# Kernel optimization log

Measured on AMD Instinct MI355X. Metric: run time of the kernel, lower is better.

Reference implementation:

```python
import jax, jax.numpy as jnp
import numpy as np

# Model dims (see init_kwargs / shape_source)
ROWS, COLS, C, K, L = 16, 16, 16, 3, 2
B, T = 16, 128
D = ROWS * COLS * C  # state_dim = 4096
PAD = (K - 1) // 2


def setup_inputs() -> dict:
    key = jax.random.key(0)
    ks = jax.random.split(key, 1 + 5 * L)
    inp = {"x_flat": jax.random.normal(ks[0], (B, T, ROWS * COLS), jnp.float32)}
    ki = 1
    for l in range(L):
        cin = (1 if l == 0 else C) + C  # conv sees concat(input, h)
        inp[f"conv_w{l}"] = jax.random.normal(ks[ki], (4 * C, cin, K), jnp.float32) * float(1.0 / np.sqrt(cin * K)); ki += 1
        inp[f"conv_b{l}"] = jnp.zeros((4 * C,), jnp.float32)
        s = float(1.0 / np.sqrt(D))
        inp[f"wq{l}"] = jax.random.normal(ks[ki], (D, D), jnp.float32) * s; ki += 1
        inp[f"wk{l}"] = jax.random.normal(ks[ki], (D, D), jnp.float32) * s; ki += 1
        inp[f"wv{l}"] = jax.random.normal(ks[ki], (D, D), jnp.float32) * s; ki += 1
        inp[f"wo{l}"] = jax.random.normal(ks[ki], (2 * D, D), jnp.float32) * float(1.0 / np.sqrt(2 * D)); ki += 1
    return inp


def _cell_step(x, h, c, cw, cb):
    # x: (B, ROWS, cin_x, COLS); h, c: (B, ROWS, C, COLS). Row-shared Conv1d
    # along cols over concat(x, h) -> 4C gates (standard ConvLSTM).
    z = jnp.concatenate([x, h], axis=2)
    z = z.reshape(B * ROWS, z.shape[2], COLS)
    g = jax.lax.conv_general_dilated(
        z, cw, window_strides=(1,), padding=[(PAD, PAD)],
        dimension_numbers=("NCH", "OIH", "NCH"))
    g = g.reshape(B, ROWS, 4 * C, COLS) + cb[None, None, :, None]
    i, f, gg, o = jnp.split(g, 4, axis=2)
    c_new = jax.nn.sigmoid(f) * c + jax.nn.sigmoid(i) * jnp.tanh(gg)
    h_new = jax.nn.sigmoid(o) * jnp.tanh(c_new)
    return h_new, c_new


def _attn_step(h_vec, kbuf, vbuf, step, wq, wo):
    # Causal dot-product attention: query from raw state, keys from raw
    # history, values from refined history (projections cached in kbuf/vbuf).
    q = h_vec @ wq                                        # (B, D)
    scores = jnp.einsum("bd,tbd->bt", q, kbuf) * (1.0 / np.sqrt(D))
    mask = (jnp.arange(T)[None, :] < step)                # (1, T) strictly-past
    scores = jnp.where(mask, scores, -1e30)
    m = jnp.max(scores, axis=1, keepdims=True)
    e = jnp.exp(scores - m) * mask
    w = e / jnp.maximum(e.sum(axis=1, keepdims=True), 1e-9)
    ctx = jnp.einsum("bt,tbd->bd", w, vbuf)               # zeros at step 0
    out = jnp.tanh(jnp.concatenate([h_vec, ctx], axis=1) @ wo)
    return out, w


def _forward(x_flat, layer_params):
    # frames: (T, B, ROWS, 1, COLS) -- matches torch view+unsqueeze(3)
    x = x_flat.reshape(B, T, ROWS, 1, COLS).transpose(1, 0, 2, 3, 4)
    h0 = tuple(jnp.zeros((B, ROWS, C, COLS), x_flat.dtype) for _ in range(L))
    kb0 = tuple(jnp.zeros((T, B, D), x_flat.dtype) for _ in range(L))

    def body(carry, x_t):
        hs, cs, kbs, vbs, s = carry
        inp = x_t
        nh, nc, nk, nv = [], [], [], []
        out = None
        for l in range(L):
            cw, cb, wq, wk, wv, wo = layer_params[l]
            h_raw, c_new = _cell_step(inp, hs[l], cs[l], cw, cb)
            h_vec = h_raw.reshape(B, D)
            out, _w = _attn_step(h_vec, kbs[l], vbs[l], s, wq, wo)
            nk.append(kbs[l].at[s].set(h_vec @ wk))   # append raw key
            nv.append(vbs[l].at[s].set(out @ wv))     # append refined value
            nh.append(h_raw); nc.append(c_new)
            inp = out.reshape(B, ROWS, C, COLS)
        return (tuple(nh), tuple(nc), tuple(nk), tuple(nv), s + 1), out

    init = (h0, h0, kb0, kb0, jnp.int32(0))
    _, outs = jax.lax.scan(body, init, x)
    return outs.transpose(1, 0, 2)  # (B, T, D) encoder outputs


def reference(x_flat, conv_w0, conv_b0, wq0, wk0, wv0, wo0,
              conv_w1, conv_b1, wq1, wk1, wv1, wo1):
    layer_params = [
        (conv_w0, conv_b0, wq0, wk0, wv0, wo0),
        (conv_w1, conv_b1, wq1, wk1, wv1, wo1),
    ]
    return _forward(x_flat, layer_params)
```

## Files before the change

kernel.cpp:

```cpp
#include <hip/hip_runtime.h>

typedef unsigned short u16;
typedef unsigned int u32;
typedef __attribute__((ext_vector_type(8))) short short8v;
typedef __attribute__((ext_vector_type(4))) float f32x4;
typedef __attribute__((ext_vector_type(8))) u16 ush8;
typedef __attribute__((ext_vector_type(4))) u16 ush4;

__device__ __forceinline__ u16 f2bf(float x) {
  u32 u = __builtin_bit_cast(u32, x);
  return (u16)((u + 0x7FFFu + ((u >> 16) & 1u)) >> 16);
}
__device__ __forceinline__ float bf2f(u16 h) {
  u32 u = ((u32)h) << 16;
  return __builtin_bit_cast(float, u);
}
__device__ __forceinline__ float sigm(float x) { return 1.f / (1.f + expf(-x)); }

typedef const __attribute__((address_space(1))) void gv_t;
typedef __attribute__((address_space(3))) void lv_t;
__device__ __forceinline__ void gload16(const void* g, void* l) {
  __builtin_amdgcn_global_load_lds((gv_t*)g, (lv_t*)l, 16, 0, 0);
}

__device__ __forceinline__ u32 ldsc32(const u32* p) {
  u32 v;
  asm volatile("global_load_dword %0, %1, off sc0 sc1\n\ts_waitcnt vmcnt(0)"
               : "=v"(v) : "v"(p) : "memory");
  return v;
}
__device__ __forceinline__ void atomswap32(u32* p, u32 v) {
  asm volatile("global_atomic_swap %0, %1, off" :: "v"(p), "v"(v) : "memory");
}

__global__ __launch_bounds__(256) void k_conv(int cin, int xmode,
    const float* __restrict__ xin, const float* __restrict__ cw,
    const float* __restrict__ cb, u16* __restrict__ hhi, u16* __restrict__ hlo)
{
  __shared__ float zb[32 * 18];
  __shared__ __align__(16) float wb[6144];
  __shared__ float bb[64];
  const int tid = threadIdx.x;
  const int b = blockIdx.x >> 4, r = blockIdx.x & 15;
  const int ch = tid >> 4, col = tid & 15;
  const int cx = cin - 16;
  for (int i = tid; i < 64 * cin * 3; i += 256) {
    int tap = i % 3, tmp = i / 3;
    int ic = tmp % cin, oc = tmp / cin;
    wb[(((oc & 15) * cin + ic) * 3 + tap) * 4 + (oc >> 4)] = cw[i];
  }
  if (tid < 64) bb[tid] = cb[tid];
  for (int i = tid; i < cin * 18; i += 256) zb[i] = 0.f;
  __syncthreads();
  float h = 0.f, c = 0.f;
  const int lane = tid & 63;
  for (int t = 0; t < 128; ++t) {
    if (xmode == 0) {
      if (ch == 0) zb[col + 1] = xin[((long)b * 128 + t) * 256 + r * 16 + col];
    } else {
      zb[ch * 18 + col + 1] = xin[((long)t * 16 + b) * 4096 + r * 256 + ch * 16 + col];
    }
    zb[(cx + ch) * 18 + col + 1] = h;
    __syncthreads();
    float a0 = bb[ch], a1 = bb[16 + ch], a2 = bb[32 + ch], a3 = bb[48 + ch];
    for (int ic = 0; ic < cin; ++ic) {
      float z1 = zb[ic * 18 + col + 1];
      float z0 = __shfl(z1, lane - 1);
      float z2 = __shfl(z1, lane + 1);
      if (col == 0) z0 = 0.f;
      if (col == 15) z2 = 0.f;
      const float4* wp = (const float4*)&wb[(ch * cin + ic) * 12];
      float4 w0 = wp[0], w1 = wp[1], w2 = wp[2];
      a0 += z0 * w0.x + z1 * w1.x + z2 * w2.x;
      a1 += z0 * w0.y + z1 * w1.y + z2 * w2.y;
      a2 += z0 * w0.z + z1 * w1.z + z2 * w2.z;
      a3 += z0 * w0.w + z1 * w1.w + z2 * w2.w;
    }
    __syncthreads();
    c = sigm(a1) * c + sigm(a0) * tanhf(a2);
    h = sigm(a3) * tanhf(c);
    long idx = ((long)t * 16 + b) * 4096 + (long)r * 256 + ch * 16 + col;
    u16 hh = f2bf(h);
    hhi[idx] = hh;
    hlo[idx] = f2bf(h - bf2f(hh));
  }
}

__global__ __launch_bounds__(256) void k_tsplit3(
    const float* __restrict__ W0, const float* __restrict__ W1,
    const float* __restrict__ W2, u16* __restrict__ hi, u16* __restrict__ lo)
{
  __shared__ float tb[32][33];
  const int y = blockIdx.y;
  const float* W = (y == 0) ? W0 : (y == 1) ? W1 : W2;
  u16* hid = hi + (unsigned long)y * 16777216UL;
  u16* lod = lo + (unsigned long)y * 16777216UL;
  const int tn = blockIdx.x & 127, tk = blockIdx.x >> 7;
  const int n0 = tn * 32, k0 = tk * 32;
  const int lr = threadIdx.x >> 5, lc = threadIdx.x & 31;
  #pragma unroll
  for (int i = 0; i < 4; ++i)
    tb[lr + i * 8][lc] = W[(long)(k0 + lr + i * 8) * 4096 + n0 + lc];
  __syncthreads();
  #pragma unroll
  for (int i = 0; i < 4; ++i) {
    int n = lr + i * 8;
    float v = tb[lc][n];
    long idx = (long)(n0 + n) * 4096 + k0 + lc;
    u16 h = f2bf(v);
    hid[idx] = h;
    lod[idx] = f2bf(v - bf2f(h));
  }
}

__global__ __launch_bounds__(256) void k_prepB2(
    const float* __restrict__ Woc, const float* __restrict__ Wv,
    u16* __restrict__ thi, u16* __restrict__ tlo,
    u16* __restrict__ vhi, u16* __restrict__ vlo)
{
  if (blockIdx.y == 1) {
    long i = ((long)blockIdx.x * 256 + threadIdx.x) * 4;
    const float4 v = *(const float4*)&Wv[i];
    u16 h0 = f2bf(v.x), h1 = f2bf(v.y), h2 = f2bf(v.z), h3 = f2bf(v.w);
    ush4 hv = {h0, h1, h2, h3};
    ush4 lv = {f2bf(v.x - bf2f(h0)), f2bf(v.y - bf2f(h1)),
               f2bf(v.z - bf2f(h2)), f2bf(v.w - bf2f(h3))};
    *(ush4*)&vhi[i] = hv;
    *(ush4*)&vlo[i] = lv;
    return;
  }
  __shared__ float tb[32][33];
  const int tn = blockIdx.x & 127, tk = blockIdx.x >> 7;
  const int n0 = tn * 32, k0 = tk * 32;
  const int lr = threadIdx.x >> 5, lc = threadIdx.x & 31;
  #pragma unroll
  for (int i = 0; i < 4; ++i)
    tb[lr + i * 8][lc] = Woc[(long)(k0 + lr + i * 8) * 4096 + n0 + lc];
  __syncthreads();
  #pragma unroll
  for (int i = 0; i < 4; ++i) {
    int n = lr + i * 8;
    float v = tb[lc][n];
    long idx = (long)(n0 + n) * 4096 + k0 + lc;
    u16 h = f2bf(v);
    thi[idx] = h;
    tlo[idx] = f2bf(v - bf2f(h));
  }
}

__global__ __launch_bounds__(256) void k_scores(
    const u16* __restrict__ Ahi, long lda, long aBS,
    const u16* __restrict__ Bhi, long ldb, long bBS,
    float* __restrict__ Sp)
{
  __shared__ __align__(16) u16 lds[2][16384];
  const int tid = threadIdx.x;
  const int lane = tid & 63;
  const int wv = tid >> 6;
  const long aOff = (long)blockIdx.y * aBS;
  const long bOff = (long)blockIdx.y * bBS;
  const long cOff = (long)blockIdx.y * 16384 + (long)blockIdx.z * 262144;
  const int kbase = blockIdx.z * 512;

  const int l8 = lane >> 3;
  const int cslot = (lane & 7) ^ l8;
  const int ck = (cslot & 3) * 8;
  const u16* aSrc = Ahi + aOff + (wv * 32 + l8) * lda + ck;
  const u16* bSrc = Bhi + bOff + (wv * 32 + l8) * ldb + ck;
  const int ldsAo = wv * 2048;
  const int ldsBo = 8192 + wv * 2048;

  const int r15 = lane & 15, kq = lane >> 4;
  const int s7 = r15 & 7;
  const int oHi = (kq ^ s7) * 8;
  const int aQ = (wv >> 1) * 64;
  const int bQ = (wv & 1) * 64;

  f32x4 acc[4][4] = {};

#define STAGE(buf, kofs)                                                     \
  {                                                                          \
    const u16* sa = aSrc + (kofs);                                           \
    const u16* sb = bSrc + (kofs);                                           \
    u16* la = &lds[buf][ldsAo];                                              \
    u16* lb = &lds[buf][ldsBo];                                              \
    gload16(sa,            la);        gload16(sa +  8 * lda, la + 512);     \
    gload16(sa + 16 * lda, la + 1024); gload16(sa + 24 * lda, la + 1536);    \
    gload16(sb,            lb);        gload16(sb +  8 * ldb, lb + 512);     \
    gload16(sb + 16 * ldb, lb + 1024); gload16(sb + 24 * ldb, lb + 1536);    \
  }

  STAGE(0, kbase)
  __syncthreads();
  int cur = 0;
  for (int k0 = kbase; k0 < kbase + 512; k0 += 32) {
    if (k0 + 32 < kbase + 512) STAGE(cur ^ 1, k0 + 32)
    const u16* L = &lds[cur][0];
    short8v bh[4];
    #pragma unroll
    for (int j = 0; j < 4; ++j)
      bh[j] = *(const short8v*)&L[8192 + (bQ + j * 16 + r15) * 64 + oHi];
    #pragma unroll
    for (int i = 0; i < 4; ++i) {
      short8v ah = *(const short8v*)&L[(aQ + i * 16 + r15) * 64 + oHi];
      #pragma unroll
      for (int j = 0; j < 4; ++j)
        acc[i][j] = __builtin_amdgcn_mfma_f32_16x16x32_bf16(ah, bh[j], acc[i][j], 0, 0, 0);
    }
    __syncthreads();
    cur ^= 1;
  }
#undef STAGE
  const long row0 = aQ, col0 = bQ;
  #pragma unroll
  for (int i = 0; i < 4; ++i)
    #pragma unroll
    for (int j = 0; j < 4; ++j) {
      long rr = row0 + i * 16 + kq * 4;
      long cc = col0 + j * 16 + r15;
      #pragma unroll
      for (int g = 0; g < 4; ++g)
        Sp[cOff + (rr + g) * 128 + cc] = acc[i][j][g];
    }
}

template<int NM, bool LOOUT>
__global__ __launch_bounds__(512) void k_gemm256(
    const u16* __restrict__ Ahi, const u16* __restrict__ Alo,
    const u16* __restrict__ Bhi, const u16* __restrict__ Blo,
    u16* __restrict__ Chi, u16* __restrict__ Clo, long ldc, int nTc)
{
  __shared__ __align__(16) u16 lds[73728];
  const int tid = threadIdx.x, lane = tid & 63, wv = tid >> 6;
  const int nwg = gridDim.x;
  const int bid2 = (blockIdx.x & 7) * (nwg >> 3) + (blockIdx.x >> 3);
  const int nT = bid2 % nTc, mT = bid2 / nTc;
  const long aRow0 = (long)mT * 256, bRow0 = (long)nT * 128;

  const int l8 = lane >> 3, cslot = (lane & 7) ^ l8, ck = (cslot & 3) * 8;
  const u16* aSrc = ((cslot < 4) ? Ahi : Alo) + (aRow0 + wv * 32 + l8) * 4096 + ck;
  const u16* bSrc = ((cslot < 4) ? Bhi : Blo) + (bRow0 + wv * 16 + l8) * 4096 + ck;
  const int laO = wv * 2048;
  const int lbO = 16384 + wv * 1024;

  const int r15 = lane & 15, kq = lane >> 4, s7 = r15 & 7;
  const int oHi = (kq ^ s7) * 8, oLo = ((4 + kq) ^ s7) * 8;
  const int wm = wv >> 1, wn = wv & 1;
  f32x4 acc[4][4] = {};

#define STG(buf, kofs)                                                       \
  {                                                                          \
    const u16* sa = aSrc + (kofs);                                           \
    const u16* sb = bSrc + (kofs);                                           \
    u16* la = &lds[(buf) * 24576 + laO];                                     \
    u16* lb = &lds[(buf) * 24576 + lbO];                                     \
    gload16(sa,             la);       gload16(sa +  8 * 4096, la + 512);    \
    gload16(sa + 16 * 4096, la + 1024); gload16(sa + 24 * 4096, la + 1536);  \
    gload16(sb,             lb);       gload16(sb +  8 * 4096, lb + 512);    \
  }

  STG(0, 0) STG(1, 32)
  for (int kt = 0; kt < 128; ++kt) {
    if (kt < 127) { asm volatile("s_waitcnt vmcnt(6)" ::: "memory"); }
    else          { asm volatile("s_waitcnt vmcnt(0)" ::: "memory"); }
    __builtin_amdgcn_sched_barrier(0);
    __builtin_amdgcn_s_barrier();
    const int bb = (kt % 3) * 24576;
    if (kt < 126) STG((kt + 2) % 3, (kt + 2) * 32)
    short8v ah[4], al[4], bh[4], bl[4];
    #pragma unroll
    for (int j = 0; j < 4; ++j) {
      int rb = bb + 16384 + (wn * 64 + j * 16 + r15) * 64;
      bh[j] = *(const short8v*)&lds[rb + oHi];
      if (NM >= 3) bl[j] = *(const short8v*)&lds[rb + oLo];
    }
    #pragma unroll
    for (int i = 0; i < 4; ++i) {
      int ra = bb + (wm * 64 + i * 16 + r15) * 64;
      ah[i] = *(const short8v*)&lds[ra + oHi];
      if (NM >= 2) al[i] = *(const short8v*)&lds[ra + oLo];
    }
    #pragma unroll
    for (int i = 0; i < 4; ++i)
      #pragma unroll
      for (int j = 0; j < 4; ++j) {
        acc[i][j] = __builtin_amdgcn_mfma_f32_16x16x32_bf16(ah[i], bh[j], acc[i][j], 0, 0, 0);
        if (NM >= 3) acc[i][j] = __builtin_amdgcn_mfma_f32_16x16x32_bf16(ah[i], bl[j], acc[i][j], 0, 0, 0);
        if (NM >= 2) acc[i][j] = __builtin_amdgcn_mfma_f32_16x16x32_bf16(al[i], bh[j], acc[i][j], 0, 0, 0);
      }
  }
#undef STG
  const long row0 = aRow0 + wm * 64;
  const long col0 = bRow0 + wn * 64;
  #pragma unroll
  for (int i = 0; i < 4; ++i)
    #pragma unroll
    for (int j = 0; j < 4; ++j) {
      long rr = row0 + i * 16 + kq * 4;
      long cc = col0 + j * 16 + r15;
      #pragma unroll
      for (int g = 0; g < 4; ++g) {
        float v = acc[i][j][g];
        long idx = (rr + g) * ldc + cc;
        u16 h = f2bf(v);
        Chi[idx] = h;
        if (LOOUT) Clo[idx] = f2bf(v - bf2f(h));
      }
    }
}

__global__ __launch_bounds__(256) void k_softmax(const float* __restrict__ Sp,
    float* __restrict__ Wx, u32* __restrict__ flags)
{
  if (blockIdx.x == 0) atomswap32(&flags[threadIdx.x * 16], 0);
  const int wv = threadIdx.x >> 6, lane = threadIdx.x & 63;
  const int idx = blockIdx.x * 4 + wv;
  const int b = idx >> 7, t = idx & 127;
  const float* row = &Sp[(long)idx * 128];
  float s0 = 0.f, s1 = 0.f;
  #pragma unroll
  for (int s = 0; s < 8; ++s) {
    s0 += row[s * 262144 + lane];
    s1 += row[s * 262144 + lane + 64];
  }
  float v0 = (lane < t) ? s0 * 0.015625f : -1e30f;
  float v1 = (lane + 64 < t) ? s1 * 0.015625f : -1e30f;
  float m = fmaxf(v0, v1);
  #pragma unroll
  for (int off = 32; off; off >>= 1) m = fmaxf(m, __shfl_xor(m, off));
  float e0 = (lane < t) ? expf(v0 - m) : 0.f;
  float e1 = (lane + 64 < t) ? expf(v1 - m) : 0.f;
  float s = e0 + e1;
  #pragma unroll
  for (int off = 32; off; off >>= 1) s += __shfl_xor(s, off);
  float inv = 1.f / fmaxf(s, 1e-9f);
  float* wr = &Wx[((long)t * 16 + b) * 128];
  wr[lane] = e0 * inv;
  wr[lane + 64] = e1 * inv;
}

__global__ __launch_bounds__(512) void k_phaseC(
    const u16* __restrict__ Wvh, const u16* __restrict__ Wvl,
    const float* __restrict__ Wx,
    const u16* __restrict__ hoh, const u16* __restrict__ hol,
    u16* __restrict__ ring_h,
    float* __restrict__ fdest, int dmode, u32* __restrict__ flags)
{
  __shared__ float VO_lds[128 * 256];
  __shared__ float vo_w[8][256];
  __shared__ float pctx0[256], pctx1[256];
  const int tid = threadIdx.x;
  const int lane = tid & 63, wv = tid >> 6;
  const int n0 = blockIdx.x * 16;
  const int r15 = lane & 15, kq = lane >> 4;
  const long kb = (long)wv * 512 + kq * 8;

  short8v Bh[16], Bl[16];
  {
    const u16* bh = Wvh + (long)(n0 + r15) * 4096 + kb;
    const u16* bl = Wvl + (long)(n0 + r15) * 4096 + kb;
    #pragma unroll
    for (int c = 0; c < 16; ++c) {
      Bh[c] = *(const short8v*)(bh + c * 32);
      Bl[c] = *(const short8v*)(bl + c * 32);
    }
    #pragma unroll
    for (int c = 0; c < 16; ++c) {
      asm volatile("" : "+v"(Bh[c]));
      asm volatile("" : "+v"(Bl[c]));
    }
  }
  const long abase = (long)r15 * 4096 + kb;
  const int b8 = tid >> 4, col8 = tid & 15;

#define GBAR_PCTX(n, T)                                                      \
  {                                                                          \
    asm volatile("s_waitcnt vmcnt(0)" ::: "memory");                         \
    __syncthreads();                                                         \
    if (tid == 0) atomswap32(&flags[(u32)blockIdx.x * 16], (n));             \
    if (tid >= 256) {                                                        \
      const int id = tid - 256;                                              \
      const int bm = id >> 4;                                                \
      const float* wrowm = &Wx[((long)((T) + 1) * 16 + bm) * 128];           \
      float c0 = 0.f, c1 = 0.f;                                              \
      int tp = 0;                                                            \
      for (; tp + 1 < (T); tp += 2) {                                        \
        c0 += wrowm[tp] * VO_lds[tp * 256 + id];                             \
        c1 += wrowm[tp + 1] * VO_lds[(tp + 1) * 256 + id];                   \
      }                                                                      \
      if (tp < (T)) c0 += wrowm[tp] * VO_lds[tp * 256 + id];                 \
      pctx0[id] = c0; pctx1[id] = c1;                                        \
    } else {                                                                 \
      while (ldsc32(&flags[tid * 16]) < (n)) __builtin_amdgcn_s_sleep(1);    \
    }                                                                        \
    __syncthreads();                                                         \
  }

#define RING_STORE(slot, oval)                                               \
  {                                                                          \
    u16 hh_ = f2bf(oval);                                                    \
    u32 vh_ = hh_;                                                           \
    u32 ph_ = (u32)__shfl_xor((int)vh_, 1);                                  \
    if (!(col8 & 1)) {                                                       \
      long oi_ = (long)(slot) * 65536 + (long)b8 * 4096 + n0 + col8;         \
      atomswap32((u32*)&ring_h[oi_], vh_ | (ph_ << 16));                     \
    }                                                                        \
  }

  if (tid < 256) {
    float v = tanhf(bf2f(hoh[(long)b8 * 12288 + n0 + col8])
                  + bf2f(hol[(long)b8 * 12288 + n0 + col8]));
    RING_STORE(0, v)
    if (dmode == 0) fdest[(long)b8 * 4096 + n0 + col8] = v;
    else            fdest[(long)b8 * 128 * 4096 + n0 + col8] = v;
  }
  u32 bn = 1;
  GBAR_PCTX(bn, 0) ++bn;

#define MF(a, b) acc = __builtin_amdgcn_mfma_f32_16x16x32_bf16(a, b, acc, 0, 0, 0);

  for (int t = 0; t < 127; ++t) {
    const u16* ph = ring_h + (long)t * 65536 + abase;
    short8v xh[16];
    #pragma unroll
    for (int c = 0; c < 16; ++c) xh[c] = *(const short8v*)(ph + c * 32);
    f32x4 acc = {0.f, 0.f, 0.f, 0.f};
    #pragma unroll
    for (int c = 0; c < 16; ++c) { MF(xh[c], Bh[c]) MF(xh[c], Bl[c]) }
    #pragma unroll
    for (int g = 0; g < 4; ++g)
      vo_w[wv][(kq * 4 + g) * 16 + r15] = acc[g];
    __syncthreads();
    if (tid < 256) {
      float v = vo_w[0][tid] + vo_w[1][tid] + vo_w[2][tid] + vo_w[3][tid]
              + vo_w[4][tid] + vo_w[5][tid] + vo_w[6][tid] + vo_w[7][tid];
      VO_lds[t * 256 + tid] = v;
      const float* wrow = &Wx[((long)(t + 1) * 16 + b8) * 128];
      long hix = ((long)(t + 1) * 16 + b8) * 12288 + n0 + col8;
      float o = tanhf(bf2f(hoh[hix]) + bf2f(hol[hix])
                      + pctx0[tid] + pctx1[tid] + wrow[t] * v);
      RING_STORE(t + 1, o)
      if (dmode == 0) fdest[((long)(t + 1) * 16 + b8) * 4096 + n0 + col8] = o;
      else            fdest[((long)b8 * 128 + (t + 1)) * 4096 + n0 + col8] = o;
    }
    if (t < 126) { GBAR_PCTX(bn, t + 1) ++bn; }
  }
#undef GBAR_PCTX
#undef RING_STORE
#undef MF
}

extern "C" void kernel_launch(void* const* d_in, const int* in_sizes, int n_in,
                              void* d_out, int out_size, void* d_ws, size_t ws_size,
                              hipStream_t stream)
{
  (void)in_sizes; (void)n_in; (void)out_size;
  if (ws_size < 472383488UL) return;
  char* ws = (char*)d_ws;
  u16* WT_hi = (u16*)(ws + 0UL);
  u16* WT_lo = (u16*)(ws + 100663296UL);
  u16* WV_hi = (u16*)(ws + 33554432UL);
  u16* WV_lo = (u16*)(ws + 134217728UL);
  u16* QKOh  = (u16*)(ws + 201326592UL);
  u16* QKOl  = (u16*)(ws + 251658240UL);
  u16* Wvo_hi = (u16*)(ws + 301989888UL);
  u16* Wvo_lo = (u16*)(ws + 335544320UL);
  u16* Hs_hi = (u16*)(ws + 369098752UL);
  u16* Hs_lo = (u16*)(ws + 385875968UL);
  float* Wmx  = (float*)(ws + 403701760UL);
  float* OUT0 = (float*)(ws + 404754432UL);
  u16* ring_h = (u16*)(ws + 438308864UL);
  float* Sp   = (float*)(ws + 455086080UL);
  u32* flg    = (u32*)(ws + 471859200UL);
  float* dout = (float*)d_out;
  const float* x_flat = (const float*)d_in[0];

  for (int l = 0; l < 2; ++l) {
    const float* cw = (const float*)d_in[1 + l * 6];
    const float* cb = (const float*)d_in[2 + l * 6];
    const float* wq = (const float*)d_in[3 + l * 6];
    const float* wk = (const float*)d_in[4 + l * 6];
    const float* wv = (const float*)d_in[5 + l * 6];
    const float* wo = (const float*)d_in[6 + l * 6];
    const int cin = (l == 0) ? 17 : 32;

    hipLaunchKernelGGL(k_conv, dim3(256), dim3(256), 0, stream,
        cin, l, (l == 0) ? x_flat : OUT0, cw, cb, Hs_hi, Hs_lo);

    hipLaunchKernelGGL(k_tsplit3, dim3(16384, 3), dim3(256), 0, stream,
        wq, wk, wo, WT_hi, WT_lo);
    hipLaunchKernelGGL((k_gemm256<1, false>), dim3(512), dim3(512), 0, stream,
        Hs_hi, Hs_hi, WT_hi, WT_hi, QKOh, (u16*)nullptr, 12288L, 64);
    hipLaunchKernelGGL((k_gemm256<3, true>), dim3(256), dim3(512), 0, stream,
        Hs_hi, Hs_lo, WT_hi + 33554432UL, WT_lo + 33554432UL,
        QKOh + 8192, QKOl + 8192, 12288L, 32);

    hipLaunchKernelGGL(k_prepB2, dim3(16384, 2), dim3(256), 0, stream,
        wo + 16777216UL, wv, WT_hi, WT_lo, WV_hi, WV_lo);
    hipLaunchKernelGGL((k_gemm256<2, true>), dim3(512), dim3(512), 0, stream,
        WT_hi, WT_lo, WV_hi, WV_hi, Wvo_hi, Wvo_lo, 4096L, 32);

    hipLaunchKernelGGL(k_scores, dim3(1, 16, 8), dim3(256), 0, stream,
        QKOh, 12288L, 196608L, QKOh + 4096, 12288L, 196608L, Sp);
    hipLaunchKernelGGL(k_softmax, dim3(512), dim3(256), 0, stream, Sp, Wmx, flg);

    hipLaunchKernelGGL(k_phaseC, dim3(256), dim3(512), 0, stream,
        Wvo_hi, Wvo_lo, Wmx, QKOh + 8192, QKOl + 8192,
        ring_h, (l == 0) ? OUT0 : dout, l, flg);
  }
}
```

Baseline: 4.083 ms.

## Fuse conv and weight-prep kernels, merge three GEMMs into one launch

Runs the ConvLSTM recurrence and all weight transpose/bf16-split preprocessing in a single k_prep launch, with the serial conv blocks (low indices) overlapping the bandwidth-bound weight conversion. The three hi/lo bf16 GEMMs are combined into one k_gemmB launch dispatched by block index. Unused lo halves of Wq/Wk/Wv are no longer written, and the HO lo buffer is compacted to a 4096 stride, which cuts memory traffic and workspace. The cost is a very large heterogeneous grid where the 256 long-running conv blocks may become the tail. OUT0 and Sp now share the same workspace region, which relies on OUT0 being fully consumed before k_scores writes Sp.

```diff
diff --git a/kernel.cpp b/kernel.cpp
--- a/kernel.cpp
+++ b/kernel.cpp
@@ -33,71 +33,101 @@
   asm volatile("global_atomic_swap %0, %1, off" :: "v"(p), "v"(v) : "memory");
 }
 
-__global__ __launch_bounds__(256) void k_conv(int cin, int xmode,
-    const float* __restrict__ xin, const float* __restrict__ cw,
-    const float* __restrict__ cb, u16* __restrict__ hhi, u16* __restrict__ hlo)
-{
-  __shared__ float zb[32 * 18];
-  __shared__ __align__(16) float wb[6144];
-  __shared__ float bb[64];
+__global__ __launch_bounds__(256) void k_prep(int cin, int xmode,
+    const float* __restrict__ xin,
+    const float* __restrict__ cw, const float* __restrict__ cb,
+    const float* __restrict__ wq, const float* __restrict__ wk,
+    const float* __restrict__ wo, const float* __restrict__ wv,
+    u16* __restrict__ hhi, u16* __restrict__ hlo,
+    u16* __restrict__ WT_hi, u16* __restrict__ WTh_lo,
+    u16* __restrict__ WTc_hi, u16* __restrict__ WTc_lo,
+    u16* __restrict__ WV_hi)
+{
+  __shared__ __align__(16) float smem[6912];
+  const int bx = blockIdx.x;
   const int tid = threadIdx.x;
-  const int b = blockIdx.x >> 4, r = blockIdx.x & 15;
-  const int ch = tid >> 4, col = tid & 15;
-  const int cx = cin - 16;
-  for (int i = tid; i < 64 * cin * 3; i += 256) {
-    int tap = i % 3, tmp = i / 3;
-    int ic = tmp % cin, oc = tmp / cin;
-    wb[(((oc & 15) * cin + ic) * 3 + tap) * 4 + (oc >> 4)] = cw[i];
-  }
-  if (tid < 64) bb[tid] = cb[tid];
-  for (int i = tid; i < cin * 18; i += 256) zb[i] = 0.f;
-  __syncthreads();
-  float h = 0.f, c = 0.f;
-  const int lane = tid & 63;
-  for (int t = 0; t < 128; ++t) {
-    if (xmode == 0) {
-      if (ch == 0) zb[col + 1] = xin[((long)b * 128 + t) * 256 + r * 16 + col];
-    } else {
-      zb[ch * 18 + col + 1] = xin[((long)t * 16 + b) * 4096 + r * 256 + ch * 16 + col];
-    }
-    zb[(cx + ch) * 18 + col + 1] = h;
+
+  if (bx < 256) {
+    float* zb = smem;
+    float* wb = smem + 576;
+    float* bb = smem + 6720;
+    const int b = bx >> 4, r = bx & 15;
+    const int ch = tid >> 4, col = tid & 15;
+    const int cx = cin - 16;
+    for (int i = tid; i < 64 * cin * 3; i += 256) {
+      int tap = i % 3, tmp = i / 3;
+      int ic = tmp % cin, oc = tmp / cin;
+      wb[(((oc & 15) * cin + ic) * 3 + tap) * 4 + (oc >> 4)] = cw[i];
+    }
+    if (tid < 64) bb[tid] = cb[tid];
+    for (int i = tid; i < cin * 18; i += 256) zb[i] = 0.f;
     __syncthreads();
-    float a0 = bb[ch], a1 = bb[16 + ch], a2 = bb[32 + ch], a3 = bb[48 + ch];
-    for (int ic = 0; ic < cin; ++ic) {
-      float z1 = zb[ic * 18 + col + 1];
-      float z0 = __shfl(z1, lane - 1);
-      float z2 = __shfl(z1, lane + 1);
-      if (col == 0) z0 = 0.f;
-      if (col == 15) z2 = 0.f;
-      const float4* wp = (const float4*)&wb[(ch * cin + ic) * 12];
-      float4 w0 = wp[0], w1 = wp[1], w2 = wp[2];
-      a0 += z0 * w0.x + z1 * w1.x + z2 * w2.x;
-      a1 += z0 * w0.y + z1 * w1.y + z2 * w2.y;
-      a2 += z0 * w0.z + z1 * w1.z + z2 * w2.z;
-      a3 += z0 * w0.w + z1 * w1.w + z2 * w2.w;
-    }
-    __syncthreads();
-    c = sigm(a1) * c + sigm(a0) * tanhf(a2);
-    h = sigm(a3) * tanhf(c);
-    long idx = ((long)t * 16 + b) * 4096 + (long)r * 256 + ch * 16 + col;
-    u16 hh = f2bf(h);
-    hhi[idx] = hh;
-    hlo[idx] = f2bf(h - bf2f(hh));
-  }
-}
-
-__global__ __launch_bounds__(256) void k_tsplit3(
-    const float* __restrict__ W0, const float* __restrict__ W1,
-    const float* __restrict__ W2, u16* __restrict__ hi, u16* __restrict__ lo)
-{
-  __shared__ float tb[32][33];
-  const int y = blockIdx.y;
-  const float* W = (y == 0) ? W0 : (y == 1) ? W1 : W2;
-  u16* hid = hi + (unsigned long)y * 16777216UL;
-  u16* lod = lo + (unsigned long)y * 16777216UL;
-  const int tn = blockIdx.x & 127, tk = blockIdx.x >> 7;
+    float h = 0.f, c = 0.f;
+    const int lane = tid & 63;
+    for (int t = 0; t < 128; ++t) {
+      if (xmode == 0) {
+        if (ch == 0) zb[col + 1] = xin[((long)b * 128 + t) * 256 + r * 16 + col];
+      } else {
+        zb[ch * 18 + col + 1] = xin[((long)t * 16 + b) * 4096 + r * 256 + ch * 16 + col];
+      }
+      zb[(cx + ch) * 18 + col + 1] = h;
+      __syncthreads();
+      float a0 = bb[ch], a1 = bb[16 + ch], a2 = bb[32 + ch], a3 = bb[48 + ch];
+      for (int ic = 0; ic < cin; ++ic) {
+        float z1 = zb[ic * 18 + col + 1];
+        float z0 = __shfl(z1, lane - 1);
+        float z2 = __shfl(z1, lane + 1);
+        if (col == 0) z0 = 0.f;
+        if (col == 15) z2 = 0.f;
+        const float4* wp = (const float4*)&wb[(ch * cin + ic) * 12];
+        float4 w0 = wp[0], w1 = wp[1], w2 = wp[2];
+        a0 += z0 * w0.x + z1 * w1.x + z2 * w2.x;
+        a1 += z0 * w0.y + z1 * w1.y + z2 * w2.y;
+        a2 += z0 * w0.z + z1 * w1.z + z2 * w2.z;
+        a3 += z0 * w0.w + z1 * w1.w + z2 * w2.w;
+      }
+      __syncthreads();
+      c = sigm(a1) * c + sigm(a0) * tanhf(a2);
+      h = sigm(a3) * tanhf(c);
+      long idx = ((long)t * 16 + b) * 4096 + (long)r * 256 + ch * 16 + col;
+      u16 hh = f2bf(h);
+      hhi[idx] = hh;
+      hlo[idx] = f2bf(h - bf2f(hh));
+    }
+    return;
+  }
+
+  if (bx >= 65792) {
+    long i = ((long)(bx - 65792) * 256 + tid) * 4;
+    const float4 v = *(const float4*)&wv[i];
+    ush4 hv = {f2bf(v.x), f2bf(v.y), f2bf(v.z), f2bf(v.w)};
+    *(ush4*)&WV_hi[i] = hv;
+    return;
+  }
+
+  float (*tb)[33] = (float(*)[33])smem;
+  const float* W;
+  u16 *hid, *lod;
+  int writeLo;
+  int tile;
+  if (bx < 49408) {
+    int t = bx - 256;
+    int y = t >> 14;
+    tile = t & 16383;
+    W = (y == 0) ? wq : (y == 1) ? wk : wo;
+    hid = WT_hi + (unsigned long)y * 16777216UL;
+    lod = WTh_lo;
+    writeLo = (y == 2);
+  } else {
+    tile = bx - 49408;
+    W = wo + 16777216UL;
+    hid = WTc_hi;
+    lod = WTc_lo;
+    writeLo = 1;
+  }
+  const int tn = tile & 127, tk = tile >> 7;
   const int n0 = tn * 32, k0 = tk * 32;
-  const int lr = threadIdx.x >> 5, lc = threadIdx.x & 31;
+  const int lr = tid >> 5, lc = tid & 31;
   #pragma unroll
   for (int i = 0; i < 4; ++i)
     tb[lr + i * 8][lc] = W[(long)(k0 + lr + i * 8) * 4096 + n0 + lc];
@@ -109,42 +139,113 @@
     long idx = (long)(n0 + n) * 4096 + k0 + lc;
     u16 h = f2bf(v);
     hid[idx] = h;
-    lod[idx] = f2bf(v - bf2f(h));
-  }
-}
-
-__global__ __launch_bounds__(256) void k_prepB2(
-    const float* __restrict__ Woc, const float* __restrict__ Wv,
-    u16* __restrict__ thi, u16* __restrict__ tlo,
-    u16* __restrict__ vhi, u16* __restrict__ vlo)
-{
-  if (blockIdx.y == 1) {
-    long i = ((long)blockIdx.x * 256 + threadIdx.x) * 4;
-    const float4 v = *(const float4*)&Wv[i];
-    u16 h0 = f2bf(v.x), h1 = f2bf(v.y), h2 = f2bf(v.z), h3 = f2bf(v.w);
-    ush4 hv = {h0, h1, h2, h3};
-    ush4 lv = {f2bf(v.x - bf2f(h0)), f2bf(v.y - bf2f(h1)),
-               f2bf(v.z - bf2f(h2)), f2bf(v.w - bf2f(h3))};
-    *(ush4*)&vhi[i] = hv;
-    *(ush4*)&vlo[i] = lv;
-    return;
-  }
-  __shared__ float tb[32][33];
-  const int tn = blockIdx.x & 127, tk = blockIdx.x >> 7;
-  const int n0 = tn * 32, k0 = tk * 32;
-  const int lr = threadIdx.x >> 5, lc = threadIdx.x & 31;
+    if (writeLo) lod[idx] = f2bf(v - bf2f(h));
+  }
+}
+
+template<int NM, bool LOOUT>
+__device__ __forceinline__ void gemm_core(u16* lds, int bid, int nwg,
+    const u16* __restrict__ Ahi, const u16* __restrict__ Alo,
+    const u16* __restrict__ Bhi, const u16* __restrict__ Blo,
+    u16* __restrict__ Chi, u16* __restrict__ Clo,
+    long ldc, long ldclo, int nTc)
+{
+  const int tid = threadIdx.x, lane = tid & 63, wv = tid >> 6;
+  const int bid2 = (bid & 7) * (nwg >> 3) + (bid >> 3);
+  const int nT = bid2 % nTc, mT = bid2 / nTc;
+  const long aRow0 = (long)mT * 256, bRow0 = (long)nT * 128;
+
+  const int l8 = lane >> 3, cslot = (lane & 7) ^ l8, ck = (cslot & 3) * 8;
+  const u16* aSrc = ((cslot < 4) ? Ahi : Alo) + (aRow0 + wv * 32 + l8) * 4096 + ck;
+  const u16* bSrc = ((cslot < 4) ? Bhi : Blo) + (bRow0 + wv * 16 + l8) * 4096 + ck;
+  const int laO = wv * 2048;
+  const int lbO = 16384 + wv * 1024;
+
+  const int r15 = lane & 15, kq = lane >> 4, s7 = r15 & 7;
+  const int oHi = (kq ^ s7) * 8, oLo = ((4 + kq) ^ s7) * 8;
+  const int wm = wv >> 1, wn = wv & 1;
+  f32x4 acc[4][4] = {};
+
+#define STG(buf, kofs)                                                       \
+  {                                                                          \
+    const u16* sa = aSrc + (kofs);                                           \
+    const u16* sb = bSrc + (kofs);                                           \
+    u16* la = &lds[(buf) * 24576 + laO];                                     \
+    u16* lb = &lds[(buf) * 24576 + lbO];                                     \
+    gload16(sa,             la);       gload16(sa +  8 * 4096, la + 512);    \
+    gload16(sa + 16 * 4096, la + 1024); gload16(sa + 24 * 4096, la + 1536);  \
+    gload16(sb,             lb);       gload16(sb +  8 * 4096, lb + 512);    \
+  }
+
+  STG(0, 0) STG(1, 32)
+  for (int kt = 0; kt < 128; ++kt) {
+    if (kt < 127) { asm volatile("s_waitcnt vmcnt(6)" ::: "memory"); }
+    else          { asm volatile("s_waitcnt vmcnt(0)" ::: "memory"); }
+    __builtin_amdgcn_sched_barrier(0);
+    __builtin_amdgcn_s_barrier();
+    const int bb = (kt % 3) * 24576;
+    if (kt < 126) STG((kt + 2) % 3, (kt + 2) * 32)
+    short8v ah[4], al[4], bh[4], bl[4];
+    #pragma unroll
+    for (int j = 0; j < 4; ++j) {
+      int rb = bb + 16384 + (wn * 64 + j * 16 + r15) * 64;
+      bh[j] = *(const short8v*)&lds[rb + oHi];
+      if (NM >= 3) bl[j] = *(const short8v*)&lds[rb + oLo];
+    }
+    #pragma unroll
+    for (int i = 0; i < 4; ++i) {
+      int ra = bb + (wm * 64 + i * 16 + r15) * 64;
+      ah[i] = *(const short8v*)&lds[ra + oHi];
+      if (NM >= 2) al[i] = *(const short8v*)&lds[ra + oLo];
+    }
+    #pragma unroll
+    for (int i = 0; i < 4; ++i)
+      #pragma unroll
+      for (int j = 0; j < 4; ++j) {
+        acc[i][j] = __builtin_amdgcn_mfma_f32_16x16x32_bf16(ah[i], bh[j], acc[i][j], 0, 0, 0);
+        if (NM >= 3) acc[i][j] = __builtin_amdgcn_mfma_f32_16x16x32_bf16(ah[i], bl[j], acc[i][j], 0, 0, 0);
+        if (NM >= 2) acc[i][j] = __builtin_amdgcn_mfma_f32_16x16x32_bf16(al[i], bh[j], acc[i][j], 0, 0, 0);
+      }
+  }
+#undef STG
+  const long row0 = aRow0 + wm * 64;
+  const long col0 = bRow0 + wn * 64;
   #pragma unroll
   for (int i = 0; i < 4; ++i)
-    tb[lr + i * 8][lc] = Woc[(long)(k0 + lr + i * 8) * 4096 + n0 + lc];
-  __syncthreads();
-  #pragma unroll
-  for (int i = 0; i < 4; ++i) {
-    int n = lr + i * 8;
-    float v = tb[lc][n];
-    long idx = (long)(n0 + n) * 4096 + k0 + lc;
-    u16 h = f2bf(v);
-    thi[idx] = h;
-    tlo[idx] = f2bf(v - bf2f(h));
+    #pragma unroll
+    for (int j = 0; j < 4; ++j) {
+      long rr = row0 + i * 16 + kq * 4;
+      long cc = col0 + j * 16 + r15;
+      #pragma unroll
+      for (int g = 0; g < 4; ++g) {
+        float v = acc[i][j][g];
+        u16 h = f2bf(v);
+        Chi[(rr + g) * ldc + cc] = h;
+        if (LOOUT) Clo[(rr + g) * ldclo + cc] = f2bf(v - bf2f(h));
+      }
+    }
+}
+
+__global__ __launch_bounds__(512) void k_gemmB(
+    const u16* __restrict__ Hs_hi, const u16* __restrict__ Hs_lo,
+    const u16* __restrict__ WT_hi, const u16* __restrict__ WTh_lo,
+    const u16* __restrict__ WTc_hi, const u16* __restrict__ WTc_lo,
+    const u16* __restrict__ WV_hi,
+    u16* __restrict__ QKOh, u16* __restrict__ HOlo,
+    u16* __restrict__ Wvo_hi, u16* __restrict__ Wvo_lo)
+{
+  __shared__ __align__(16) u16 lds[73728];
+  const int bx = blockIdx.x;
+  if (bx < 512) {
+    gemm_core<1, false>(lds, bx, 512, Hs_hi, Hs_hi, WT_hi, WT_hi,
+                        QKOh, (u16*)nullptr, 12288L, 0L, 64);
+  } else if (bx < 768) {
+    gemm_core<3, true>(lds, bx - 512, 256, Hs_hi, Hs_lo,
+                       WT_hi + 33554432UL, WTh_lo,
+                       QKOh + 8192, HOlo, 12288L, 4096L, 32);
+  } else {
+    gemm_core<2, true>(lds, bx - 768, 512, WTc_hi, WTc_lo, WV_hi, WV_hi,
+                       Wvo_hi, Wvo_lo, 4096L, 4096L, 32);
   }
 }
 
@@ -221,91 +322,6 @@
       #pragma unroll
       for (int g = 0; g < 4; ++g)
         Sp[cOff + (rr + g) * 128 + cc] = acc[i][j][g];
-    }
-}
-
-template<int NM, bool LOOUT>
-__global__ __launch_bounds__(512) void k_gemm256(
-    const u16* __restrict__ Ahi, const u16* __restrict__ Alo,
-    const u16* __restrict__ Bhi, const u16* __restrict__ Blo,
-    u16* __restrict__ Chi, u16* __restrict__ Clo, long ldc, int nTc)
-{
-  __shared__ __align__(16) u16 lds[73728];
-  const int tid = threadIdx.x, lane = tid & 63, wv = tid >> 6;
-  const int nwg = gridDim.x;
-  const int bid2 = (blockIdx.x & 7) * (nwg >> 3) + (blockIdx.x >> 3);
-  const int nT = bid2 % nTc, mT = bid2 / nTc;
-  const long aRow0 = (long)mT * 256, bRow0 = (long)nT * 128;
-
-  const int l8 = lane >> 3, cslot = (lane & 7) ^ l8, ck = (cslot & 3) * 8;
-  const u16* aSrc = ((cslot < 4) ? Ahi : Alo) + (aRow0 + wv * 32 + l8) * 4096 + ck;
-  const u16* bSrc = ((cslot < 4) ? Bhi : Blo) + (bRow0 + wv * 16 + l8) * 4096 + ck;
-  const int laO = wv * 2048;
-  const int lbO = 16384 + wv * 1024;
-
-  const int r15 = lane & 15, kq = lane >> 4, s7 = r15 & 7;
-  const int oHi = (kq ^ s7) * 8, oLo = ((4 + kq) ^ s7) * 8;
-  const int wm = wv >> 1, wn = wv & 1;
-  f32x4 acc[4][4] = {};
-
-#define STG(buf, kofs)                                                       \
-  {                                                                          \
-    const u16* sa = aSrc + (kofs);                                           \
-    const u16* sb = bSrc + (kofs);                                           \
-    u16* la = &lds[(buf) * 24576 + laO];                                     \
-    u16* lb = &lds[(buf) * 24576 + lbO];                                     \
-    gload16(sa,             la);       gload16(sa +  8 * 4096, la + 512);    \
-    gload16(sa + 16 * 4096, la + 1024); gload16(sa + 24 * 4096, la + 1536);  \
-    gload16(sb,             lb);       gload16(sb +  8 * 4096, lb + 512);    \
-  }
-
-  STG(0, 0) STG(1, 32)
-  for (int kt = 0; kt < 128; ++kt) {
-    if (kt < 127) { asm volatile("s_waitcnt vmcnt(6)" ::: "memory"); }
-    else          { asm volatile("s_waitcnt vmcnt(0)" ::: "memory"); }
-    __builtin_amdgcn_sched_barrier(0);
-    __builtin_amdgcn_s_barrier();
-    const int bb = (kt % 3) * 24576;
-    if (kt < 126) STG((kt + 2) % 3, (kt + 2) * 32)
-    short8v ah[4], al[4], bh[4], bl[4];
-    #pragma unroll
-    for (int j = 0; j < 4; ++j) {
-      int rb = bb + 16384 + (wn * 64 + j * 16 + r15) * 64;
-      bh[j] = *(const short8v*)&lds[rb + oHi];
-      if (NM >= 3) bl[j] = *(const short8v*)&lds[rb + oLo];
-    }
-    #pragma unroll
-    for (int i = 0; i < 4; ++i) {
-      int ra = bb + (wm * 64 + i * 16 + r15) * 64;
-      ah[i] = *(const short8v*)&lds[ra + oHi];
-      if (NM >= 2) al[i] = *(const short8v*)&lds[ra + oLo];
-    }
-    #pragma unroll
-    for (int i = 0; i < 4; ++i)
-      #pragma unroll
-      for (int j = 0; j < 4; ++j) {
-        acc[i][j] = __builtin_amdgcn_mfma_f32_16x16x32_bf16(ah[i], bh[j], acc[i][j], 0, 0, 0);
-        if (NM >= 3) acc[i][j] = __builtin_amdgcn_mfma_f32_16x16x32_bf16(ah[i], bl[j], acc[i][j], 0, 0, 0);
-        if (NM >= 2) acc[i][j] = __builtin_amdgcn_mfma_f32_16x16x32_bf16(al[i], bh[j], acc[i][j], 0, 0, 0);
-      }
-  }
-#undef STG
-  const long row0 = aRow0 + wm * 64;
-  const long col0 = bRow0 + wn * 64;
-  #pragma unroll
-  for (int i = 0; i < 4; ++i)
-    #pragma unroll
-    for (int j = 0; j < 4; ++j) {
-      long rr = row0 + i * 16 + kq * 4;
-      long cc = col0 + j * 16 + r15;
-      #pragma unroll
-      for (int g = 0; g < 4; ++g) {
-        float v = acc[i][j][g];
-        long idx = (rr + g) * ldc + cc;
-        u16 h = f2bf(v);
-        Chi[idx] = h;
-        if (LOOUT) Clo[idx] = f2bf(v - bf2f(h));
-      }
     }
 }
 
@@ -409,7 +425,7 @@
 
   if (tid < 256) {
     float v = tanhf(bf2f(hoh[(long)b8 * 12288 + n0 + col8])
-                  + bf2f(hol[(long)b8 * 12288 + n0 + col8]));
+                  + bf2f(hol[(long)b8 * 4096 + n0 + col8]));
     RING_STORE(0, v)
     if (dmode == 0) fdest[(long)b8 * 4096 + n0 + col8] = v;
     else            fdest[(long)b8 * 128 * 4096 + n0 + col8] = v;
@@ -436,9 +452,9 @@
               + vo_w[4][tid] + vo_w[5][tid] + vo_w[6][tid] + vo_w[7][tid];
       VO_lds[t * 256 + tid] = v;
       const float* wrow = &Wx[((long)(t + 1) * 16 + b8) * 128];
-      long hix = ((long)(t + 1) * 16 + b8) * 12288 + n0 + col8;
-      float o = tanhf(bf2f(hoh[hix]) + bf2f(hol[hix])
-                      + pctx0[tid] + pctx1[tid] + wrow[t] * v);
+      float ho = bf2f(hoh[((long)(t + 1) * 16 + b8) * 12288 + n0 + col8])
+               + bf2f(hol[((long)(t + 1) * 16 + b8) * 4096 + n0 + col8]);
+      float o = tanhf(ho + pctx0[tid] + pctx1[tid] + wrow[t] * v);
       RING_STORE(t + 1, o)
       if (dmode == 0) fdest[((long)(t + 1) * 16 + b8) * 4096 + n0 + col8] = o;
       else            fdest[((long)b8 * 128 + (t + 1)) * 4096 + n0 + col8] = o;
@@ -455,23 +471,24 @@
                               hipStream_t stream)
 {
   (void)in_sizes; (void)n_in; (void)out_size;
-  if (ws_size < 472383488UL) return;
+  if (ws_size < 454049792UL) return;
   char* ws = (char*)d_ws;
-  u16* WT_hi = (u16*)(ws + 0UL);
-  u16* WT_lo = (u16*)(ws + 100663296UL);
-  u16* WV_hi = (u16*)(ws + 33554432UL);
-  u16* WV_lo = (u16*)(ws + 134217728UL);
-  u16* QKOh  = (u16*)(ws + 201326592UL);
-  u16* QKOl  = (u16*)(ws + 251658240UL);
+  u16* WT_hi  = (u16*)(ws + 0UL);
+  u16* WTh_lo = (u16*)(ws + 100663296UL);
+  u16* WTc_hi = (u16*)(ws + 134217728UL);
+  u16* WTc_lo = (u16*)(ws + 167772160UL);
+  u16* WV_hi  = (u16*)(ws + 201326592UL);
+  u16* QKOh   = (u16*)(ws + 234881024UL);
+  u16* HOlo   = (u16*)(ws + 285212672UL);
   u16* Wvo_hi = (u16*)(ws + 301989888UL);
   u16* Wvo_lo = (u16*)(ws + 335544320UL);
-  u16* Hs_hi = (u16*)(ws + 369098752UL);
-  u16* Hs_lo = (u16*)(ws + 385875968UL);
-  float* Wmx  = (float*)(ws + 403701760UL);
-  float* OUT0 = (float*)(ws + 404754432UL);
-  u16* ring_h = (u16*)(ws + 438308864UL);
-  float* Sp   = (float*)(ws + 455086080UL);
-  u32* flg    = (u32*)(ws + 471859200UL);
+  u16* Hs_hi  = (u16*)(ws + 369098752UL);
+  u16* Hs_lo  = (u16*)(ws + 385875968UL);
+  float* Wmx  = (float*)(ws + 402653184UL);
+  u16* ring_h = (u16*)(ws + 403701760UL);
+  float* OUT0 = (float*)(ws + 420478976UL);
+  float* Sp   = (float*)(ws + 420478976UL);
+  u32* flg    = (u32*)(ws + 454033408UL);
   float* dout = (float*)d_out;
   const float* x_flat = (const float*)d_in[0];
 
@@ -484,28 +501,20 @@
     const float* wo = (const float*)d_in[6 + l * 6];
     const int cin = (l == 0) ? 17 : 32;
 
-    hipLaunchKernelGGL(k_conv, dim3(256), dim3(256), 0, stream,
-        cin, l, (l == 0) ? x_flat : OUT0, cw, cb, Hs_hi, Hs_lo);
-
-    hipLaunchKernelGGL(k_tsplit3, dim3(16384, 3), dim3(256), 0, stream,
-        wq, wk, wo, WT_hi, WT_lo);
-    hipLaunchKernelGGL((k_gemm256<1, false>), dim3(512), dim3(512), 0, stream,
-        Hs_hi, Hs_hi, WT_hi, WT_hi, QKOh, (u16*)nullptr, 12288L, 64);
-    hipLaunchKernelGGL((k_gemm256<3, true>), dim3(256), dim3(512), 0, stream,
-        Hs_hi, Hs_lo, WT_hi + 33554432UL, WT_lo + 33554432UL,
-        QKOh + 8192, QKOl + 8192, 12288L, 32);
-
-    hipLaunchKernelGGL(k_prepB2, dim3(16384, 2), dim3(256), 0, stream,
-        wo + 16777216UL, wv, WT_hi, WT_lo, WV_hi, WV_lo);
-    hipLaunchKernelGGL((k_gemm256<2, true>), dim3(512), dim3(512), 0, stream,
-        WT_hi, WT_lo, WV_hi, WV_hi, Wvo_hi, Wvo_lo, 4096L, 32);
+    hipLaunchKernelGGL(k_prep, dim3(82176), dim3(256), 0, stream,
+        cin, l, (l == 0) ? x_flat : OUT0, cw, cb, wq, wk, wo, wv,
+        Hs_hi, Hs_lo, WT_hi, WTh_lo, WTc_hi, WTc_lo, WV_hi);
+
+    hipLaunchKernelGGL(k_gemmB, dim3(1280), dim3(512), 0, stream,
+        Hs_hi, Hs_lo, WT_hi, WTh_lo, WTc_hi, WTc_lo, WV_hi,
+        QKOh, HOlo, Wvo_hi, Wvo_lo);
 
     hipLaunchKernelGGL(k_scores, dim3(1, 16, 8), dim3(256), 0, stream,
         QKOh, 12288L, 196608L, QKOh + 4096, 12288L, 196608L, Sp);
     hipLaunchKernelGGL(k_softmax, dim3(512), dim3(256), 0, stream, Sp, Wmx, flg);
 
     hipLaunchKernelGGL(k_phaseC, dim3(256), dim3(512), 0, stream,
-        Wvo_hi, Wvo_lo, Wmx, QKOh + 8192, QKOl + 8192,
+        Wvo_hi, Wvo_lo, Wmx, QKOh + 8192, HOlo,
         ring_h, (l == 0) ? OUT0 : dout, l, flg);
   }
 }
```

Result: faster. 3.893 ms (-4.6%).
